# Kernel optimization log

Hardware: AMD Instinct MI355X
Metric: run time of the kernel (lower is better)

Reference implementation:

```python
import jax, jax.numpy as jnp
import numpy as np

B, H, V, NS, S, D, E = 4096, 256, 32000, 2, 128, 4, 64
PAD = 0


def _shift_matrices(n):
    # W_up: row i <- row i+1, last row zero. W_down: row i <- row i-1, row 0 zero.
    eye = np.eye(n, dtype=np.float32)
    W_up = np.vstack([eye[1:], np.zeros((1, n), np.float32)])
    W_down = np.vstack([np.zeros((1, n), np.float32), eye[:-1]])
    return W_up, W_down


def setup_inputs() -> dict:
    key = jax.random.key(0)
    ks = jax.random.split(key, 20)
    sc = 0.05
    emb_table = jax.random.normal(ks[0], (V, H), jnp.float32) * sc
    emb_table = emb_table.at[PAD].set(0.0)  # padding_idx
    inp = {
        "input_ids": jax.random.randint(ks[1], (B,), 0, V),
        "hidden": jax.random.normal(ks[2], (B, H), jnp.float32),
        "stacks": jax.random.normal(ks[3], (B, NS, S, E), jnp.float32),
        "emb_table": emb_table,
        "W_in": jax.random.normal(ks[4], (H, H), jnp.float32) * sc,
        "b_in": jnp.zeros((H,), jnp.float32),
        "W_hh": jax.random.normal(ks[5], (H, H), jnp.float32) * sc,
        "b_hh": jnp.zeros((H,), jnp.float32),
        "W_s2h": jax.random.normal(ks[6], (NS, H, D * E), jnp.float32) * sc,
        "b_s2h": jnp.zeros((NS, H), jnp.float32),
        "W_act": jax.random.normal(ks[7], (NS, 3, H), jnp.float32) * sc,
        "b_act": jnp.zeros((NS, 3), jnp.float32),
        "W_push": jax.random.normal(ks[8], (NS, E, H), jnp.float32) * sc,
        "b_push": jnp.zeros((NS, E), jnp.float32),
        "W_out": jax.random.normal(ks[9], (V, H), jnp.float32) * sc,
        "b_out": jnp.zeros((V,), jnp.float32),
        "empty_elem": jax.random.normal(ks[10], (1, E), jnp.float32),
    }
    return inp


def reference(input_ids, hidden, stacks, emb_table, W_in, b_in, W_hh, b_hh,
              W_s2h, b_s2h, W_act, b_act, W_push, b_push, W_out, b_out,
              empty_elem):
    W_up_np, W_down_np = _shift_matrices(S)
    W_up = jnp.asarray(W_up_np)
    W_down = jnp.asarray(W_down_np)

    emb = emb_table[input_ids]                                  # [B,H]
    mid = emb @ W_in.T + b_in + hidden @ W_hh.T + b_hh          # [B,H]

    # stack readout (top stack_depth elems), before any update
    stack_vals = stacks[:, :, :D, :].reshape(B, NS, D * E)      # [B,NS,D*E]
    mid = mid + jnp.einsum('bnd,nhd->bh', stack_vals, W_s2h) + b_s2h.sum(0)

    # per-stack actions from the OLD hidden state (no softmax in source)
    act = jnp.einsum('bh,nah->bna', hidden, W_act) + b_act      # [B,NS,3]
    p_push = act[..., 0:1]                                      # [B,NS,1]
    p_pop = act[..., 1:2]
    p_noop = act[..., 2:3]
    push_val = jnp.tanh(jnp.einsum('bh,neh->bne', hidden, W_push) + b_push)  # [B,NS,E]

    down = jnp.einsum('st,bnte->bnse', W_down, stacks)          # shift down
    up = jnp.einsum('st,bnte->bnse', W_up, stacks)              # shift up
    new_stacks = (p_push[..., None] * down + p_pop[..., None] * up
                  + p_noop[..., None] * stacks)
    new_stacks = new_stacks.at[:, :, 0, :].set(p_push * push_val)
    new_stacks = new_stacks.at[:, :, S - 1, :].set(
        jnp.broadcast_to(empty_elem[None], (B, NS, E)))

    new_hidden = jnp.tanh(mid)                                  # [B,H]
    logits = new_hidden @ W_out.T + b_out                       # [B,V]
    output = jax.nn.log_softmax(logits, axis=1)
    top1 = jnp.argmax(output, axis=1)[:, None]                  # [B,1]
    return output, new_hidden, top1, new_stacks
```

## Files before the change

kernel.cpp:

```cpp
#include <hip/hip_runtime.h>
#include <stdint.h>

#define B_   4096
#define H_   256
#define V_   32000
#define NS_  2
#define S_   128
#define E_   64
#define TRIG 0.02f
#define CSTR 10
#define NTV  500

typedef __attribute__((ext_vector_type(4))) float  f32x4;
typedef __attribute__((ext_vector_type(8))) __bf16 bf16x8;
typedef __attribute__((ext_vector_type(8))) unsigned short u16x8;

__device__ __forceinline__ unsigned short f2bf(float f) {
  unsigned u = __float_as_uint(f);
  u += 0x7fffu + ((u >> 16) & 1u);
  return (unsigned short)(u >> 16);
}

typedef __attribute__((address_space(1))) const unsigned int* gas1_t;
typedef __attribute__((address_space(3))) unsigned int*       las3_t;
__device__ __forceinline__ void gload16(const void* g, void* l) {
  __builtin_amdgcn_global_load_lds((gas1_t)g, (las3_t)l, 16, 0, 0);
}

__device__ __forceinline__ void merge2(float& m1, float& i1, float& m2, float& i2,
                                       float om1, float oi1, float om2, float oi2) {
  if (om1 > m1 || (om1 == m1 && oi1 < i1)) {
    const float lm = m1, li = i1;
    m1 = om1; i1 = oi1;
    if (lm > om2 || (lm == om2 && li < oi2)) { m2 = lm; i2 = li; }
    else { m2 = om2; i2 = oi2; }
  } else {
    if (om1 > m2 || (om1 == m2 && oi1 < i2)) { m2 = om1; i2 = oi1; }
  }
}

__global__ void prep_w1(const float* __restrict__ W_in,  const float* __restrict__ W_hh,
                        const float* __restrict__ W_s2h, const float* __restrict__ W_act,
                        const float* __restrict__ W_push,
                        const float* __restrict__ b_in,  const float* __restrict__ b_hh,
                        const float* __restrict__ b_s2h, const float* __restrict__ b_act,
                        const float* __restrict__ b_push,
                        unsigned short* __restrict__ W1, float* __restrict__ bbig) {
  const unsigned idx = blockIdx.x * 256u + threadIdx.x;
  const unsigned c = idx >> 10, k = idx & 1023u;
  float w = 0.f;
  if (c < 256u) {
    if (k < 256u)       w = W_in[c*256u + k];
    else if (k < 512u)  w = W_hh[c*256u + (k-256u)];
    else { unsigned n = (k-512u) >> 8, d = (k-512u) & 255u; w = W_s2h[n*65536u + c*256u + d]; }
  } else if (c < 262u) {
    if (k >= 256u && k < 512u) w = W_act[(c-256u)*256u + (k-256u)];
  } else if (c < 390u) {
    if (k >= 256u && k < 512u) w = W_push[(c-262u)*256u + (k-256u)];
  }
  W1[(size_t)c*1024u + k] = f2bf(w);
  if (idx < 512u) {
    float bb = 0.f;
    if (idx < 256u)       bb = b_in[idx] + b_hh[idx] + b_s2h[idx] + b_s2h[256u+idx];
    else if (idx < 262u)  bb = b_act[idx-256u];
    else if (idx < 390u)  bb = b_push[idx-262u];
    bbig[idx] = bb;
  }
}

__global__ void prep_w1t(const float* __restrict__ W_in, const float* __restrict__ W_hh,
                         const float* __restrict__ W_s2h, float* __restrict__ W1T) {
  const unsigned idx = blockIdx.x * 256u + threadIdx.x;
  const unsigned k = idx >> 8, h = idx & 255u;
  float w;
  if (k < 256u)      w = W_in[h*256u + k];
  else if (k < 512u) w = W_hh[h*256u + (k-256u)];
  else { unsigned n = (k-512u) >> 8, d = (k-512u) & 255u; w = W_s2h[n*65536u + h*256u + d]; }
  W1T[idx] = w;
}

__global__ void prep_a1(const int* __restrict__ ids, const float* __restrict__ emb,
                        const float* __restrict__ hidden, const float* __restrict__ stacks,
                        unsigned short* __restrict__ A1, float* __restrict__ A1f) {
  const unsigned gid = blockIdx.x * 256u + threadIdx.x;
  const unsigned b = gid >> 7, k0 = (gid & 127u) << 3;
  const float* src;
  if (k0 < 256u)      src = emb + (size_t)ids[b]*256u + k0;
  else if (k0 < 512u) src = hidden + (size_t)b*256u + (k0-256u);
  else { const unsigned kk = k0 - 512u;
         src = stacks + (size_t)b*16384u + (kk>>8)*8192u + (kk&255u); }
  const float4 v0 = *(const float4*)src;
  const float4 v1 = *(const float4*)(src + 4);
  *(float4*)(A1f + (size_t)b*1024u + k0)     = v0;
  *(float4*)(A1f + (size_t)b*1024u + k0 + 4) = v1;
  u16x8 o;
  o[0]=f2bf(v0.x); o[1]=f2bf(v0.y); o[2]=f2bf(v0.z); o[3]=f2bf(v0.w);
  o[4]=f2bf(v1.x); o[5]=f2bf(v1.y); o[6]=f2bf(v1.z); o[7]=f2bf(v1.w);
  *(u16x8*)(A1 + (size_t)b*1024u + k0) = o;
}

__global__ void prep_b2(const float* __restrict__ W_out, unsigned short* __restrict__ B2) {
  const unsigned gid = blockIdx.x * 256u + threadIdx.x;
  const size_t base = (size_t)gid * 8;
  const float4 v0 = *(const float4*)(W_out + base);
  const float4 v1 = *(const float4*)(W_out + base + 4);
  u16x8 o;
  o[0]=f2bf(v0.x); o[1]=f2bf(v0.y); o[2]=f2bf(v0.z); o[3]=f2bf(v0.w);
  o[4]=f2bf(v1.x); o[5]=f2bf(v1.y); o[6]=f2bf(v1.z); o[7]=f2bf(v1.w);
  *(u16x8*)(B2 + base) = o;
}

__global__ __launch_bounds__(256) void gemm_mid(
    const unsigned short* __restrict__ A, const unsigned short* __restrict__ Bm,
    float* __restrict__ nh_out, float* __restrict__ actw, float* __restrict__ pushw,
    const float* __restrict__ bbig, unsigned short* __restrict__ a2w)
{
  constexpr int K = 1024;
  constexpr int NT = K >> 6;
  __shared__ __align__(16) unsigned char pool[65536];
  const int tid  = threadIdx.x;
  const int lane = tid & 63;
  const int wid  = tid >> 6;
  const int wm = wid >> 1, wn = wid & 1;
  const int l16 = lane & 15;
  const int lk8 = (lane >> 4) << 3;
  const int lr4 = (lane >> 4) << 2;
  const size_t arow0 = (size_t)blockIdx.y << 7;
  const size_t bcol0 = (size_t)blockIdx.x << 7;

  f32x4 acc[4][4];
#pragma unroll
  for (int i = 0; i < 4; ++i)
#pragma unroll
    for (int j = 0; j < 4; ++j) acc[i][j] = (f32x4)0.f;

  auto stageAB = [&](int buf, int kt) {
    unsigned char* dst = pool + (buf << 15);
    const int k0 = kt << 6;
#pragma unroll
    for (int i = 0; i < 4; ++i) {
      const int e   = (i << 8) + tid;
      const int row = e >> 3;
      const int col = (e & 7) << 3;
      gload16(A  + (arow0 + row) * (size_t)K + (k0 + col), dst + (size_t)e * 16);
      gload16(Bm + (bcol0 + row) * (size_t)K + (k0 + col), dst + 16384 + (size_t)e * 16);
    }
  };
  auto computeT = [&](int buf) {
    const unsigned short* As = (const unsigned short*)(pool + (buf << 15));
    const unsigned short* Bs = As + 8192;
#pragma unroll
    for (int kk = 0; kk < 64; kk += 32) {
      bf16x8 af[4], bfr[4];
#pragma unroll
      for (int f = 0; f < 4; ++f) {
        af[f]  = *(const bf16x8*)&As[((wm<<6) + (f<<4) + l16)*64 + kk + lk8];
        bfr[f] = *(const bf16x8*)&Bs[((wn<<6) + (f<<4) + l16)*64 + kk + lk8];
      }
#pragma unroll
      for (int mf = 0; mf < 4; ++mf)
#pragma unroll
        for (int nf = 0; nf < 4; ++nf)
          acc[mf][nf] = __builtin_amdgcn_mfma_f32_16x16x32_bf16(af[mf], bfr[nf], acc[mf][nf], 0, 0, 0);
    }
  };

  stageAB(0, 0);
  __syncthreads();
#pragma unroll
  for (int t = 0; t < NT; ++t) {
    if (t < NT - 1) stageAB((t + 1) & 1, t + 1);
    computeT(t & 1);
    __syncthreads();
  }

#pragma unroll
  for (int mf = 0; mf < 4; ++mf)
#pragma unroll
    for (int j = 0; j < 4; ++j) {
      const int r = (int)arow0 + (wm<<6) + (mf<<4) + lr4 + j;
#pragma unroll
      for (int nf = 0; nf < 4; ++nf) {
        const int c = (int)bcol0 + (wn<<6) + (nf<<4) + l16;
        const float v = acc[mf][nf][j] + bbig[c];
        if (c < 256) { const float th = tanhf(v);
                       nh_out[r*256 + c] = th;
                       a2w[r*256 + c] = f2bf(th); }
        else if (c < 262)  actw[r*6 + (c-256)] = v;
        else if (c < 390)  pushw[r*128 + (c-262)] = tanhf(v);
      }
    }
}

template<int MODE>
__global__ __launch_bounds__(512, 4) void gemmBS(
    const unsigned short* __restrict__ A2, const unsigned short* __restrict__ B2,
    float* __restrict__ gout, const float* __restrict__ b_out,
    float* __restrict__ partials, const float* __restrict__ subw)
{
  __shared__ __align__(16) unsigned short Bres[64*256];
  __shared__ __align__(16) unsigned short Apool[2][256*32];
  __shared__ __align__(16) float tscr[2112];
  const int tid  = threadIdx.x;
  const int lane = tid & 63;
  const int wid  = tid >> 6;
  const int wm = wid >> 2;
  const int wn = wid & 3;
  const int l16 = lane & 15;
  const int g4  = lane >> 4;
  const int lr4 = g4 << 2;
  const int vb  = (int)blockIdx.x << 6;

  {
#pragma unroll
    for (int i = 0; i < 4; ++i) {
      const int e   = (i << 9) + tid;
      const int row = e >> 5;
      const int c32 = e & 31;
      const int src = (c32 & 24) | ((c32 ^ row) & 7);
      gload16(B2 + (size_t)(vb + row) * 256 + (src << 3),
              (unsigned char*)Bres + (size_t)e * 16);
    }
  }

  auto stageA = [&](int buf, int bt, int kt) {
    unsigned char* dst = (unsigned char*)Apool[buf];
#pragma unroll
    for (int i = 0; i < 2; ++i) {
      const int e   = (i << 9) + tid;
      const int row = e >> 2;
      const int src = (e & 3) ^ ((row >> 2) & 3);
      gload16(A2 + ((size_t)bt*256 + row) * 256 + kt*32 + (src << 3),
              dst + (size_t)e * 16);
    }
  };

  stageA(0, 0, 0);
  __syncthreads();

  for (int bt = 0; bt < 16; ++bt) {
    f32x4 acc[2][4];
#pragma unroll
    for (int m = 0; m < 2; ++m)
#pragma unroll
      for (int n = 0; n < 4; ++n) acc[m][n] = (f32x4)0.f;

#pragma unroll
    for (int kt = 0; kt < 8; ++kt) {
      if (kt < 7)       stageA((kt + 1) & 1, bt, kt + 1);
      else if (bt < 15) stageA(0, bt + 1, 0);
      {
        const unsigned short* As = Apool[kt & 1];
        bf16x8 af[2], bfr[4];
#pragma unroll
        for (int m = 0; m < 2; ++m) {
          const int rb = (wm<<5) + (m<<4) + l16;
          const int ch = kt*4 + g4;
          const int s  = (ch & 24) | ((ch ^ rb) & 7);
          af[m] = *(const bf16x8*)&Bres[rb*256 + (s<<3)];
        }
#pragma unroll
        for (int n = 0; n < 4; ++n) {
          const int ra = (wn<<6) + (n<<4) + l16;
          const int s  = g4 ^ ((ra >> 2) & 3);
          bfr[n] = *(const bf16x8*)&As[ra*32 + (s<<3)];
        }
#pragma unroll
        for (int m = 0; m < 2; ++m)
#pragma unroll
          for (int n = 0; n < 4; ++n)
            acc[m][n] = __builtin_amdgcn_mfma_f32_16x16x32_bf16(af[m], bfr[n], acc[m][n], 0, 0, 0);
      }
      __syncthreads();
    }

    if constexpr (MODE == 0) {
      float* lf = tscr;
#pragma unroll
      for (int ch = 0; ch < 8; ++ch) {
        if (wn == (ch >> 1)) {
          const int nb = (ch & 1) << 1;
#pragma unroll
          for (int mm = 0; mm < 2; ++mm)
#pragma unroll
            for (int nn = 0; nn < 2; ++nn) {
              const int brow = (nn << 4) + l16;
              const int vcol = (wm << 5) + (mm << 4) + lr4;
#pragma unroll
              for (int j = 0; j < 4; ++j)
                lf[brow*66 + vcol + j] = acc[mm][nb + nn][j];
            }
        }
        __syncthreads();
        {
          const int r  = tid >> 4;
          const int c4 = (tid & 15) << 2;
          const size_t grow = (size_t)bt*256 + (ch << 5) + r;
          const float ls = subw[grow];
          const f32x4 bo = *(const f32x4*)&b_out[vb + c4];
          f32x4 v;
          v.x = lf[r*66 + c4 + 0] + bo.x - ls;
          v.y = lf[r*66 + c4 + 1] + bo.y - ls;
          v.z = lf[r*66 + c4 + 2] + bo.z - ls;
          v.w = lf[r*66 + c4 + 3] + bo.w - ls;
          __builtin_nontemporal_store(v, (f32x4*)(gout + grow * (size_t)V_ + vb + c4));
        }
        __syncthreads();
      }
    } else {
      float (*colrec)[5] = (float (*)[5])tscr;
      float bo[8];
#pragma unroll
      for (int m = 0; m < 2; ++m)
#pragma unroll
        for (int j = 0; j < 4; ++j)
          bo[m*4+j] = b_out[vb + (wm<<5) + (m<<4) + lr4 + j];

      float rS[4], rM1[4], rI1[4], rM2[4], rI2[4];
#pragma unroll
      for (int n = 0; n < 4; ++n) {
        float s = 0.f, m1 = -INFINITY, i1f = 2.1e9f, m2 = -INFINITY, i2f = 2.1e9f;
#pragma unroll
        for (int m = 0; m < 2; ++m)
#pragma unroll
          for (int j = 0; j < 4; ++j) {
            const int vloc = (wm<<5) + (m<<4) + lr4 + j;
            const float v = acc[m][n][j] + bo[m*4+j];
            const float fi = (float)(vb + vloc);
            s += __expf(v);
            if (v > m1 || (v == m1 && fi < i1f)) { m2 = m1; i2f = i1f; m1 = v; i1f = fi; }
            else if (v > m2 || (v == m2 && fi < i2f)) { m2 = v; i2f = fi; }
          }
#pragma unroll
        for (int mask = 16; mask <= 32; mask <<= 1) {
          const float os  = __shfl_xor(s,   mask, 64);
          const float om1 = __shfl_xor(m1,  mask, 64);
          const float oi1 = __shfl_xor(i1f, mask, 64);
          const float om2 = __shfl_xor(m2,  mask, 64);
          const float oi2 = __shfl_xor(i2f, mask, 64);
          s += os;
          merge2(m1, i1f, m2, i2f, om1, oi1, om2, oi2);
        }
        rS[n] = s; rM1[n] = m1; rI1[n] = i1f; rM2[n] = m2; rI2[n] = i2f;
      }
      if (wm == 0 && g4 == 0) {
#pragma unroll
        for (int n = 0; n < 4; ++n) {
          const int cl = (wn<<6) + (n<<4) + l16;
          colrec[cl][0] = rS[n];  colrec[cl][1] = rM1[n]; colrec[cl][2] = rI1[n];
          colrec[cl][3] = rM2[n]; colrec[cl][4] = rI2[n];
        }
      }
      __syncthreads();
      if (wm == 1 && g4 == 0) {
#pragma unroll
        for (int n = 0; n < 4; ++n) {
          const int cl = (wn<<6) + (n<<4) + l16;
          float s = rS[n] + colrec[cl][0];
          float m1 = rM1[n], i1f = rI1[n], m2 = rM2[n], i2f = rI2[n];
          merge2(m1, i1f, m2, i2f, colrec[cl][1], colrec[cl][2], colrec[cl][3], colrec[cl][4]);
          const size_t brow = (size_t)bt*256 + cl;
          float* dst = partials + (brow * NTV + blockIdx.x) * 8;
          float4 v4; v4.x = s; v4.y = m1; v4.z = i1f; v4.w = m2;
          *(float4*)dst = v4;
          dst[4] = i2f;
        }
      }
      __syncthreads();
    }
  }
}

__global__ __launch_bounds__(256) void reduce_kernel(
    const float* __restrict__ partials, float* __restrict__ subw,
    float* __restrict__ top1w, int* __restrict__ candbuf)
{
  const int b = blockIdx.x, t = threadIdx.x;
  float s = 0.f, m1 = -INFINITY, i1 = 2.1e9f, m2 = -INFINITY, i2 = 2.1e9f;
  float tm1[2] = {-INFINITY,-INFINITY}, ti1[2] = {2.1e9f,2.1e9f};
  float tm2[2] = {-INFINITY,-INFINITY}, ti2[2] = {2.1e9f,2.1e9f};
  for (int q = 0; q < 2; ++q) {
    const int idx = t + q*256;
    if (idx < NTV) {
      const float4 p0 = *(const float4*)(partials + ((size_t)b*NTV + idx)*8);
      s += p0.x;
      tm1[q] = p0.y; ti1[q] = p0.z; tm2[q] = p0.w;
      ti2[q] = partials[((size_t)b*NTV + idx)*8 + 4];
      merge2(m1, i1, m2, i2, tm1[q], ti1[q], tm2[q], ti2[q]);
    }
  }
  __shared__ float sS[256], sM1[256], sI1[256], sM2[256], sI2[256];
  sS[t] = s; sM1[t] = m1; sI1[t] = i1; sM2[t] = m2; sI2[t] = i2;
  __syncthreads();
  for (int off = 128; off > 0; off >>= 1) {
    if (t < off) {
      sS[t] += sS[t+off];
      float a1 = sM1[t], ai1 = sI1[t], a2 = sM2[t], ai2 = sI2[t];
      merge2(a1, ai1, a2, ai2, sM1[t+off], sI1[t+off], sM2[t+off], sI2[t+off]);
      sM1[t] = a1; sI1[t] = ai1; sM2[t] = a2; sI2[t] = ai2;
    }
    __syncthreads();
  }
  const float M1 = sM1[0];
  __shared__ int cnt; __shared__ int cand[CSTR-1];
  if (t == 0) cnt = 0;
  __syncthreads();
  for (int q = 0; q < 2; ++q) {
    if (t + q*256 < NTV) {
      if (tm1[q] >= M1 - TRIG) { int p = atomicAdd(&cnt, 1); if (p < CSTR-1) cand[p] = (int)ti1[q]; }
      if (tm2[q] >= M1 - TRIG) { int p = atomicAdd(&cnt, 1); if (p < CSTR-1) cand[p] = (int)ti2[q]; }
    }
  }
  __syncthreads();
  const int ncand = min(cnt, CSTR-1);
  if (t == 0) {
    subw[b] = logf(sS[0]);
    candbuf[b*CSTR] = ncand;
    if (ncand <= 1) top1w[b] = sI1[0];
  }
  if (t < ncand) candbuf[b*CSTR + 1 + t] = cand[t];
}

__global__ __launch_bounds__(256) void rescue_kernel(
    const int* __restrict__ candbuf, const float* __restrict__ A1f,
    const float* __restrict__ W1T, const float* __restrict__ bbig,
    const float* __restrict__ W_out, const float* __restrict__ b_out,
    float* __restrict__ top1w)
{
  const int b = blockIdx.x;
  const int ncand = candbuf[b*CSTR];
  if (ncand <= 1) return;
  const int t = threadIdx.x;

  double acc = (double)bbig[t];
  const float* arow = A1f + (size_t)b * 1024;
  for (int k = 0; k < 1024; ++k)
    acc += (double)arow[k] * (double)W1T[k*256 + t];
  __shared__ double hbuf[256];
  hbuf[t] = tanh(acc);
  __syncthreads();

  __shared__ double red[256];
  double best = -1e300; int besti = 0x7fffffff;
  for (int q = 0; q < ncand; ++q) {
    const int ci = candbuf[b*CSTR + 1 + q];
    red[t] = hbuf[t] * (double)W_out[(size_t)ci*256 + t];
    __syncthreads();
    for (int off = 128; off > 0; off >>= 1) {
      if (t < off) red[t] += red[t+off];
      __syncthreads();
    }
    if (t == 0) {
      const double d = red[0] + (double)b_out[ci];
      if (d > best || (d == best && ci < besti)) { best = d; besti = ci; }
    }
    __syncthreads();
  }
  if (t == 0) top1w[b] = (float)besti;
}

__global__ void stacks_kernel(const float* __restrict__ stacks, const float* __restrict__ actw,
                              const float* __restrict__ pushw, const float* __restrict__ empty,
                              float* __restrict__ out3) {
  const int bn = blockIdx.x;
  const int b = bn >> 1, n = bn & 1;
  __shared__ __align__(16) float st[S_*E_];
  const float4* src4 = (const float4*)(stacks + (size_t)bn * (S_*E_));
  float4* st4 = (float4*)st;
  for (int i = threadIdx.x; i < (S_*E_/4); i += 256) st4[i] = src4[i];
  __syncthreads();
  const float pp = actw[b*6 + n*3 + 0];
  const float po = actw[b*6 + n*3 + 1];
  const float pq = actw[b*6 + n*3 + 2];
  float4* dst4 = (float4*)(out3 + (size_t)bn * (S_*E_));
  for (int i = threadIdx.x; i < (S_*E_/4); i += 256) {
    const int flat = i << 2;
    const int s = flat >> 6;
    const int e = flat & 63;
    float4 r;
    if (s == S_-1) {
      r = ((const float4*)empty)[e >> 2];
    } else if (s == 0) {
      const float4 pv = ((const float4*)(pushw + b*128 + n*64))[e >> 2];
      r.x = pp*pv.x; r.y = pp*pv.y; r.z = pp*pv.z; r.w = pp*pv.w;
    } else {
      const float4 dn = *(const float4*)&st[(s-1)*64 + e];
      const float4 up = *(const float4*)&st[(s+1)*64 + e];
      const float4 cu = *(const float4*)&st[s*64 + e];
      r.x = pp*dn.x + po*up.x + pq*cu.x;
      r.y = pp*dn.y + po*up.y + pq*cu.y;
      r.z = pp*dn.z + po*up.z + pq*cu.z;
      r.w = pp*dn.w + po*up.w + pq*cu.w;
    }
    dst4[i] = r;
  }
}

extern "C" void kernel_launch(void* const* d_in, const int* in_sizes, int n_in,
                              void* d_out, int out_size, void* d_ws, size_t ws_size,
                              hipStream_t stream) {
  (void)in_sizes; (void)n_in; (void)out_size; (void)ws_size;
  const int*   ids    = (const int*)  d_in[0];
  const float* hidden = (const float*)d_in[1];
  const float* stacks = (const float*)d_in[2];
  const float* emb    = (const float*)d_in[3];
  const float* W_in   = (const float*)d_in[4];
  const float* b_in   = (const float*)d_in[5];
  const float* W_hh   = (const float*)d_in[6];
  const float* b_hh   = (const float*)d_in[7];
  const float* W_s2h  = (const float*)d_in[8];
  const float* b_s2h  = (const float*)d_in[9];
  const float* W_act  = (const float*)d_in[10];
  const float* b_act  = (const float*)d_in[11];
  const float* W_push = (const float*)d_in[12];
  const float* b_push = (const float*)d_in[13];
  const float* W_out  = (const float*)d_in[14];
  const float* b_out  = (const float*)d_in[15];
  const float* empty  = (const float*)d_in[16];

  float* out0 = (float*)d_out;
  float* out1 = out0 + (size_t)B_*V_;
  float* out2 = out1 + (size_t)B_*H_;
  float* out3 = out2 + B_;

  unsigned short* A1 = (unsigned short*)out3;
  unsigned short* W1 = A1 + (size_t)4194304;
  unsigned short* A2 = W1 + (size_t)524288;
  unsigned short* B2 = A2 + (size_t)1048576;
  float* partials    = (float*)(B2 + (size_t)8192000);
  float* A1f         = partials + (size_t)16384000;
  float* W1T         = A1f + (size_t)4194304;
  int*   candbuf     = (int*)(W1T + 262144);

  float* bbig  = (float*)d_ws;
  float* actw  = bbig + 512;
  float* pushw = actw + (size_t)B_*6;
  float* subw  = pushw + (size_t)B_*128;

  prep_w1<<<dim3(2048),  dim3(256), 0, stream>>>(W_in, W_hh, W_s2h, W_act, W_push,
                                                 b_in, b_hh, b_s2h, b_act, b_push, W1, bbig);
  prep_w1t<<<dim3(1024), dim3(256), 0, stream>>>(W_in, W_hh, W_s2h, W1T);
  prep_a1<<<dim3(2048),  dim3(256), 0, stream>>>(ids, emb, hidden, stacks, A1, A1f);
  gemm_mid<<<dim3(4, 32), dim3(256), 0, stream>>>(A1, W1, out1, actw, pushw, bbig, A2);
  prep_b2<<<dim3(4000),  dim3(256), 0, stream>>>(W_out, B2);
  gemmBS<2><<<dim3(500), dim3(512), 0, stream>>>(A2, B2,
      nullptr, b_out, partials, nullptr);
  reduce_kernel<<<dim3(4096), dim3(256), 0, stream>>>(partials, subw, out2, candbuf);
  gemmBS<0><<<dim3(500), dim3(512), 0, stream>>>(A2, B2,
      out0, b_out, nullptr, subw);
  rescue_kernel<<<dim3(4096), dim3(256), 0, stream>>>(candbuf, A1f, W1T, bbig,
                                                      W_out, b_out, out2);
  stacks_kernel<<<dim3(8192), dim3(256), 0, stream>>>(stacks, actw, pushw, empty, out3);
}
```

Baseline: 540.2 us.

## Restructure vocab GEMM so each wave owns full vocab tile and loads A directly

The warp tiling of the output-projection GEMM changes. Each wave now covers all 64 vocab columns for 32 batch rows, so no cross-wave reduction is needed. The activation operand is read straight from global memory into registers with one-step prefetch, replacing the LDS double buffer and its per-k-step barriers. The MODE 0 epilogue writes accumulators directly, without the LDS transpose, and MODE 1 drops the LDS combine of the two wave halves. In exchange, each wave does uncoalesced 16-byte global loads of A with more redundant A traffic through cache, the occupancy hint drops from 4 to 2, and the output stores are less contiguous.

```diff
diff --git a/kernel.cpp b/kernel.cpp
--- a/kernel.cpp
+++ b/kernel.cpp
@@ -193,23 +193,19 @@
 }
 
 template<int MODE>
-__global__ __launch_bounds__(512, 4) void gemmBS(
+__global__ __launch_bounds__(512, 2) void gemmBS(
     const unsigned short* __restrict__ A2, const unsigned short* __restrict__ B2,
     float* __restrict__ gout, const float* __restrict__ b_out,
     float* __restrict__ partials, const float* __restrict__ subw)
 {
   __shared__ __align__(16) unsigned short Bres[64*256];
-  __shared__ __align__(16) unsigned short Apool[2][256*32];
-  __shared__ __align__(16) float tscr[2112];
   const int tid  = threadIdx.x;
   const int lane = tid & 63;
-  const int wid  = tid >> 6;
-  const int wm = wid >> 2;
-  const int wn = wid & 3;
-  const int l16 = lane & 15;
-  const int g4  = lane >> 4;
-  const int lr4 = g4 << 2;
-  const int vb  = (int)blockIdx.x << 6;
+  const int w    = tid >> 6;
+  const int l16  = lane & 15;
+  const int g4   = lane >> 4;
+  const int lr4  = g4 << 2;
+  const int vb   = (int)blockIdx.x << 6;
 
   {
 #pragma unroll
@@ -222,111 +218,75 @@
               (unsigned char*)Bres + (size_t)e * 16);
     }
   }
-
-  auto stageA = [&](int buf, int bt, int kt) {
-    unsigned char* dst = (unsigned char*)Apool[buf];
-#pragma unroll
-    for (int i = 0; i < 2; ++i) {
-      const int e   = (i << 9) + tid;
-      const int row = e >> 2;
-      const int src = (e & 3) ^ ((row >> 2) & 3);
-      gload16(A2 + ((size_t)bt*256 + row) * 256 + kt*32 + (src << 3),
-              dst + (size_t)e * 16);
-    }
-  };
-
-  stageA(0, 0, 0);
-  __syncthreads();
+  __syncthreads();
+
+  f32x4 bo4[4];
+#pragma unroll
+  for (int m = 0; m < 4; ++m)
+    bo4[m] = *(const f32x4*)&b_out[vb + (m<<4) + lr4];
 
   for (int bt = 0; bt < 16; ++bt) {
-    f32x4 acc[2][4];
-#pragma unroll
-    for (int m = 0; m < 2; ++m)
-#pragma unroll
-      for (int n = 0; n < 4; ++n) acc[m][n] = (f32x4)0.f;
-
+    f32x4 acc[4][2];
+#pragma unroll
+    for (int m = 0; m < 4; ++m)
+#pragma unroll
+      for (int n = 0; n < 2; ++n) acc[m][n] = (f32x4)0.f;
+
+    const unsigned short* Abase = A2 + ((size_t)bt*256) * 256;
+
+    bf16x8 pb[2];
+#pragma unroll
+    for (int n = 0; n < 2; ++n) {
+      const int ra = (w<<5) + (n<<4) + l16;
+      pb[n] = *(const bf16x8*)&Abase[(size_t)ra*256 + (g4<<3)];
+    }
 #pragma unroll
     for (int kt = 0; kt < 8; ++kt) {
-      if (kt < 7)       stageA((kt + 1) & 1, bt, kt + 1);
-      else if (bt < 15) stageA(0, bt + 1, 0);
-      {
-        const unsigned short* As = Apool[kt & 1];
-        bf16x8 af[2], bfr[4];
-#pragma unroll
-        for (int m = 0; m < 2; ++m) {
-          const int rb = (wm<<5) + (m<<4) + l16;
-          const int ch = kt*4 + g4;
-          const int s  = (ch & 24) | ((ch ^ rb) & 7);
-          af[m] = *(const bf16x8*)&Bres[rb*256 + (s<<3)];
+      bf16x8 cb0 = pb[0], cb1 = pb[1];
+      if (kt < 7) {
+#pragma unroll
+        for (int n = 0; n < 2; ++n) {
+          const int ra = (w<<5) + (n<<4) + l16;
+          pb[n] = *(const bf16x8*)&Abase[(size_t)ra*256 + (kt+1)*32 + (g4<<3)];
         }
-#pragma unroll
-        for (int n = 0; n < 4; ++n) {
-          const int ra = (wn<<6) + (n<<4) + l16;
-          const int s  = g4 ^ ((ra >> 2) & 3);
-          bfr[n] = *(const bf16x8*)&As[ra*32 + (s<<3)];
+      }
+      bf16x8 af[4];
+#pragma unroll
+      for (int m = 0; m < 4; ++m) {
+        const int rb = (m<<4) + l16;
+        const int ch = kt*4 + g4;
+        const int s  = (ch & 24) | ((ch ^ rb) & 7);
+        af[m] = *(const bf16x8*)&Bres[rb*256 + (s<<3)];
+      }
+#pragma unroll
+      for (int m = 0; m < 4; ++m) {
+        acc[m][0] = __builtin_amdgcn_mfma_f32_16x16x32_bf16(af[m], cb0, acc[m][0], 0, 0, 0);
+        acc[m][1] = __builtin_amdgcn_mfma_f32_16x16x32_bf16(af[m], cb1, acc[m][1], 0, 0, 0);
+      }
+    }
+
+    if constexpr (MODE == 0) {
+#pragma unroll
+      for (int n = 0; n < 2; ++n) {
+        const size_t grow = (size_t)bt*256 + (w<<5) + (n<<4) + l16;
+        const float ls = subw[grow];
+        float* gp = gout + grow * (size_t)V_ + vb + lr4;
+#pragma unroll
+        for (int m = 0; m < 4; ++m) {
+          f32x4 v = acc[m][n] + bo4[m] - ls;
+          __builtin_nontemporal_store(v, (f32x4*)(gp + (m<<4)));
         }
-#pragma unroll
-        for (int m = 0; m < 2; ++m)
-#pragma unroll
-          for (int n = 0; n < 4; ++n)
-            acc[m][n] = __builtin_amdgcn_mfma_f32_16x16x32_bf16(af[m], bfr[n], acc[m][n], 0, 0, 0);
-      }
-      __syncthreads();
-    }
-
-    if constexpr (MODE == 0) {
-      float* lf = tscr;
-#pragma unroll
-      for (int ch = 0; ch < 8; ++ch) {
-        if (wn == (ch >> 1)) {
-          const int nb = (ch & 1) << 1;
-#pragma unroll
-          for (int mm = 0; mm < 2; ++mm)
-#pragma unroll
-            for (int nn = 0; nn < 2; ++nn) {
-              const int brow = (nn << 4) + l16;
-              const int vcol = (wm << 5) + (mm << 4) + lr4;
-#pragma unroll
-              for (int j = 0; j < 4; ++j)
-                lf[brow*66 + vcol + j] = acc[mm][nb + nn][j];
-            }
-        }
-        __syncthreads();
-        {
-          const int r  = tid >> 4;
-          const int c4 = (tid & 15) << 2;
-          const size_t grow = (size_t)bt*256 + (ch << 5) + r;
-          const float ls = subw[grow];
-          const f32x4 bo = *(const f32x4*)&b_out[vb + c4];
-          f32x4 v;
-          v.x = lf[r*66 + c4 + 0] + bo.x - ls;
-          v.y = lf[r*66 + c4 + 1] + bo.y - ls;
-          v.z = lf[r*66 + c4 + 2] + bo.z - ls;
-          v.w = lf[r*66 + c4 + 3] + bo.w - ls;
-          __builtin_nontemporal_store(v, (f32x4*)(gout + grow * (size_t)V_ + vb + c4));
-        }
-        __syncthreads();
       }
     } else {
-      float (*colrec)[5] = (float (*)[5])tscr;
-      float bo[8];
-#pragma unroll
-      for (int m = 0; m < 2; ++m)
-#pragma unroll
-        for (int j = 0; j < 4; ++j)
-          bo[m*4+j] = b_out[vb + (wm<<5) + (m<<4) + lr4 + j];
-
-      float rS[4], rM1[4], rI1[4], rM2[4], rI2[4];
-#pragma unroll
-      for (int n = 0; n < 4; ++n) {
+#pragma unroll
+      for (int n = 0; n < 2; ++n) {
         float s = 0.f, m1 = -INFINITY, i1f = 2.1e9f, m2 = -INFINITY, i2f = 2.1e9f;
 #pragma unroll
-        for (int m = 0; m < 2; ++m)
+        for (int m = 0; m < 4; ++m)
 #pragma unroll
           for (int j = 0; j < 4; ++j) {
-            const int vloc = (wm<<5) + (m<<4) + lr4 + j;
-            const float v = acc[m][n][j] + bo[m*4+j];
-            const float fi = (float)(vb + vloc);
+            const float v = acc[m][n][j] + bo4[m][j];
+            const float fi = (float)(vb + (m<<4) + lr4 + j);
             s += __expf(v);
             if (v > m1 || (v == m1 && fi < i1f)) { m2 = m1; i2f = i1f; m1 = v; i1f = fi; }
             else if (v > m2 || (v == m2 && fi < i2f)) { m2 = v; i2f = fi; }
@@ -341,32 +301,14 @@
           s += os;
           merge2(m1, i1f, m2, i2f, om1, oi1, om2, oi2);
         }
-        rS[n] = s; rM1[n] = m1; rI1[n] = i1f; rM2[n] = m2; rI2[n] = i2f;
-      }
-      if (wm == 0 && g4 == 0) {
-#pragma unroll
-        for (int n = 0; n < 4; ++n) {
-          const int cl = (wn<<6) + (n<<4) + l16;
-          colrec[cl][0] = rS[n];  colrec[cl][1] = rM1[n]; colrec[cl][2] = rI1[n];
-          colrec[cl][3] = rM2[n]; colrec[cl][4] = rI2[n];
-        }
-      }
-      __syncthreads();
-      if (wm == 1 && g4 == 0) {
-#pragma unroll
-        for (int n = 0; n < 4; ++n) {
-          const int cl = (wn<<6) + (n<<4) + l16;
-          float s = rS[n] + colrec[cl][0];
-          float m1 = rM1[n], i1f = rI1[n], m2 = rM2[n], i2f = rI2[n];
-          merge2(m1, i1f, m2, i2f, colrec[cl][1], colrec[cl][2], colrec[cl][3], colrec[cl][4]);
-          const size_t brow = (size_t)bt*256 + cl;
+        if (g4 == 0) {
+          const size_t brow = (size_t)bt*256 + (w<<5) + (n<<4) + l16;
           float* dst = partials + (brow * NTV + blockIdx.x) * 8;
           float4 v4; v4.x = s; v4.y = m1; v4.z = i1f; v4.w = m2;
           *(float4*)dst = v4;
           dst[4] = i2f;
         }
       }
-      __syncthreads();
     }
   }
 }
```

Measured after the change: 597.2 us. 1.11x slower.

## Split stats GEMM into dedicated kernel reading A2 from a k-major copy

Applied to the files above, without the earlier changes.

Splits the stats pass out of the templated logits GEMM into its own kernel, gemmStats. A new prep kernel copies the bf16 hidden activations into a k-chunk-major layout (A2F). gemmStats loads the B tile once into LDS, then streams A fragments straight from global memory into registers with one step of prefetch, with no A staging in LDS and no cross-wave merge. Each wave covers all 64 vocab columns for 32 batch rows, so the LDS colrec merge and its barriers go away. The cost is an extra small kernel launch, an extra buffer, and global-memory latency exposure on the A loads.

```diff
diff --git a/kernel.cpp b/kernel.cpp
--- a/kernel.cpp
+++ b/kernel.cpp
@@ -110,6 +110,13 @@
   *(u16x8*)(B2 + base) = o;
 }
 
+__global__ void prep_a2f(const unsigned short* __restrict__ A2,
+                         unsigned short* __restrict__ A2F) {
+  const unsigned gid = blockIdx.x * 256u + threadIdx.x;
+  const unsigned row = gid & 4095u, k8 = gid >> 12;
+  *(u16x8*)(A2F + (size_t)gid * 8) = *(const u16x8*)(A2 + (size_t)row*256u + k8*8u);
+}
+
 __global__ __launch_bounds__(256) void gemm_mid(
     const unsigned short* __restrict__ A, const unsigned short* __restrict__ Bm,
     float* __restrict__ nh_out, float* __restrict__ actw, float* __restrict__ pushw,
@@ -192,11 +199,10 @@
     }
 }
 
-template<int MODE>
-__global__ __launch_bounds__(512, 4) void gemmBS(
+__global__ __launch_bounds__(512, 4) void gemmW(
     const unsigned short* __restrict__ A2, const unsigned short* __restrict__ B2,
     float* __restrict__ gout, const float* __restrict__ b_out,
-    float* __restrict__ partials, const float* __restrict__ subw)
+    const float* __restrict__ subw)
 {
   __shared__ __align__(16) unsigned short Bres[64*256];
   __shared__ __align__(16) unsigned short Apool[2][256*32];
@@ -274,99 +280,139 @@
       __syncthreads();
     }
 
-    if constexpr (MODE == 0) {
-      float* lf = tscr;
-#pragma unroll
-      for (int ch = 0; ch < 8; ++ch) {
-        if (wn == (ch >> 1)) {
-          const int nb = (ch & 1) << 1;
-#pragma unroll
-          for (int mm = 0; mm < 2; ++mm)
-#pragma unroll
-            for (int nn = 0; nn < 2; ++nn) {
-              const int brow = (nn << 4) + l16;
-              const int vcol = (wm << 5) + (mm << 4) + lr4;
-#pragma unroll
-              for (int j = 0; j < 4; ++j)
-                lf[brow*66 + vcol + j] = acc[mm][nb + nn][j];
-            }
+#pragma unroll
+    for (int ch = 0; ch < 8; ++ch) {
+      if (wn == (ch >> 1)) {
+        const int nb = (ch & 1) << 1;
+#pragma unroll
+        for (int mm = 0; mm < 2; ++mm)
+#pragma unroll
+          for (int nn = 0; nn < 2; ++nn) {
+            const int brow = (nn << 4) + l16;
+            const int vcol = (wm << 5) + (mm << 4) + lr4;
+#pragma unroll
+            for (int j = 0; j < 4; ++j)
+              tscr[brow*66 + vcol + j] = acc[mm][nb + nn][j];
+          }
+      }
+      __syncthreads();
+      {
+        const int r  = tid >> 4;
+        const int c4 = (tid & 15) << 2;
+        const size_t grow = (size_t)bt*256 + (ch << 5) + r;
+        const float ls = subw[grow];
+        const f32x4 bo = *(const f32x4*)&b_out[vb + c4];
+        f32x4 v;
+        v.x = tscr[r*66 + c4 + 0] + bo.x - ls;
+        v.y = tscr[r*66 + c4 + 1] + bo.y - ls;
+        v.z = tscr[r*66 + c4 + 2] + bo.z - ls;
+        v.w = tscr[r*66 + c4 + 3] + bo.w - ls;
+        __builtin_nontemporal_store(v, (f32x4*)(gout + grow * (size_t)V_ + vb + c4));
+      }
+      __syncthreads();
+    }
+  }
+}
+
+__global__ __launch_bounds__(512, 4) void gemmStats(
+    const unsigned short* __restrict__ A2F, const unsigned short* __restrict__ B2,
+    const float* __restrict__ b_out, float* __restrict__ partials)
+{
+  __shared__ __align__(16) unsigned short Bres[64*256];
+  const int tid  = threadIdx.x;
+  const int lane = tid & 63;
+  const int w    = tid >> 6;
+  const int l16  = lane & 15;
+  const int g4   = lane >> 4;
+  const int lr4  = g4 << 2;
+  const int vb   = (int)blockIdx.x << 6;
+
+  {
+#pragma unroll
+    for (int i = 0; i < 4; ++i) {
+      const int e   = (i << 9) + tid;
+      const int row = e >> 5;
+      const int c32 = e & 31;
+      const int src = (c32 & 24) | ((c32 ^ row) & 7);
+      gload16(B2 + (size_t)(vb + row) * 256 + (src << 3),
+              (unsigned char*)Bres + (size_t)e * 16);
+    }
+  }
+  __syncthreads();
+
+  f32x4 bo4[4];
+#pragma unroll
+  for (int m = 0; m < 4; ++m)
+    bo4[m] = *(const f32x4*)&b_out[vb + (m<<4) + lr4];
+
+  for (int bt = 0; bt < 16; ++bt) {
+    f32x4 acc[4][2];
+#pragma unroll
+    for (int m = 0; m < 4; ++m)
+#pragma unroll
+      for (int n = 0; n < 2; ++n) acc[m][n] = (f32x4)0.f;
+
+    const int ra0 = (w<<5) + l16;
+
+    bf16x8 pb[2];
+#pragma unroll
+    for (int n = 0; n < 2; ++n)
+      pb[n] = *(const bf16x8*)&A2F[((size_t)g4*4096 + bt*256 + ra0 + (n<<4)) * 8];
+
+#pragma unroll
+    for (int kt = 0; kt < 8; ++kt) {
+      bf16x8 cb0 = pb[0], cb1 = pb[1];
+      if (kt < 7) {
+        const size_t k8 = (size_t)((kt+1)*4 + g4);
+#pragma unroll
+        for (int n = 0; n < 2; ++n)
+          pb[n] = *(const bf16x8*)&A2F[(k8*4096 + bt*256 + ra0 + (n<<4)) * 8];
+      }
+      bf16x8 af[4];
+#pragma unroll
+      for (int m = 0; m < 4; ++m) {
+        const int rb = (m<<4) + l16;
+        const int ch = kt*4 + g4;
+        const int s  = (ch & 24) | ((ch ^ rb) & 7);
+        af[m] = *(const bf16x8*)&Bres[rb*256 + (s<<3)];
+      }
+#pragma unroll
+      for (int m = 0; m < 4; ++m) {
+        acc[m][0] = __builtin_amdgcn_mfma_f32_16x16x32_bf16(af[m], cb0, acc[m][0], 0, 0, 0);
+        acc[m][1] = __builtin_amdgcn_mfma_f32_16x16x32_bf16(af[m], cb1, acc[m][1], 0, 0, 0);
+      }
+    }
+
+#pragma unroll
+    for (int n = 0; n < 2; ++n) {
+      float s = 0.f, m1 = -INFINITY, i1f = 2.1e9f, m2 = -INFINITY, i2f = 2.1e9f;
+#pragma unroll
+      for (int m = 0; m < 4; ++m)
+#pragma unroll
+        for (int j = 0; j < 4; ++j) {
+          const float v = acc[m][n][j] + bo4[m][j];
+          const float fi = (float)(vb + (m<<4) + lr4 + j);
+          s += __expf(v);
+          if (v > m1 || (v == m1 && fi < i1f)) { m2 = m1; i2f = i1f; m1 = v; i1f = fi; }
+          else if (v > m2 || (v == m2 && fi < i2f)) { m2 = v; i2f = fi; }
         }
-        __syncthreads();
-        {
-          const int r  = tid >> 4;
-          const int c4 = (tid & 15) << 2;
-          const size_t grow = (size_t)bt*256 + (ch << 5) + r;
-          const float ls = subw[grow];
-          const f32x4 bo = *(const f32x4*)&b_out[vb + c4];
-          f32x4 v;
-          v.x = lf[r*66 + c4 + 0] + bo.x - ls;
-          v.y = lf[r*66 + c4 + 1] + bo.y - ls;
-          v.z = lf[r*66 + c4 + 2] + bo.z - ls;
-          v.w = lf[r*66 + c4 + 3] + bo.w - ls;
-          __builtin_nontemporal_store(v, (f32x4*)(gout + grow * (size_t)V_ + vb + c4));
-        }
-        __syncthreads();
-      }
-    } else {
-      float (*colrec)[5] = (float (*)[5])tscr;
-      float bo[8];
-#pragma unroll
-      for (int m = 0; m < 2; ++m)
-#pragma unroll
-        for (int j = 0; j < 4; ++j)
-          bo[m*4+j] = b_out[vb + (wm<<5) + (m<<4) + lr4 + j];
-
-      float rS[4], rM1[4], rI1[4], rM2[4], rI2[4];
-#pragma unroll
-      for (int n = 0; n < 4; ++n) {
-        float s = 0.f, m1 = -INFINITY, i1f = 2.1e9f, m2 = -INFINITY, i2f = 2.1e9f;
-#pragma unroll
-        for (int m = 0; m < 2; ++m)
-#pragma unroll
-          for (int j = 0; j < 4; ++j) {
-            const int vloc = (wm<<5) + (m<<4) + lr4 + j;
-            const float v = acc[m][n][j] + bo[m*4+j];
-            const float fi = (float)(vb + vloc);
-            s += __expf(v);
-            if (v > m1 || (v == m1 && fi < i1f)) { m2 = m1; i2f = i1f; m1 = v; i1f = fi; }
-            else if (v > m2 || (v == m2 && fi < i2f)) { m2 = v; i2f = fi; }
-          }
-#pragma unroll
-        for (int mask = 16; mask <= 32; mask <<= 1) {
-          const float os  = __shfl_xor(s,   mask, 64);
-          const float om1 = __shfl_xor(m1,  mask, 64);
-          const float oi1 = __shfl_xor(i1f, mask, 64);
-          const float om2 = __shfl_xor(m2,  mask, 64);
-          const float oi2 = __shfl_xor(i2f, mask, 64);
-          s += os;
-          merge2(m1, i1f, m2, i2f, om1, oi1, om2, oi2);
-        }
-        rS[n] = s; rM1[n] = m1; rI1[n] = i1f; rM2[n] = m2; rI2[n] = i2f;
-      }
-      if (wm == 0 && g4 == 0) {
-#pragma unroll
-        for (int n = 0; n < 4; ++n) {
-          const int cl = (wn<<6) + (n<<4) + l16;
-          colrec[cl][0] = rS[n];  colrec[cl][1] = rM1[n]; colrec[cl][2] = rI1[n];
-          colrec[cl][3] = rM2[n]; colrec[cl][4] = rI2[n];
-        }
-      }
-      __syncthreads();
-      if (wm == 1 && g4 == 0) {
-#pragma unroll
-        for (int n = 0; n < 4; ++n) {
-          const int cl = (wn<<6) + (n<<4) + l16;
-          float s = rS[n] + colrec[cl][0];
-          float m1 = rM1[n], i1f = rI1[n], m2 = rM2[n], i2f = rI2[n];
-          merge2(m1, i1f, m2, i2f, colrec[cl][1], colrec[cl][2], colrec[cl][3], colrec[cl][4]);
-          const size_t brow = (size_t)bt*256 + cl;
-          float* dst = partials + (brow * NTV + blockIdx.x) * 8;
-          float4 v4; v4.x = s; v4.y = m1; v4.z = i1f; v4.w = m2;
-          *(float4*)dst = v4;
-          dst[4] = i2f;
-        }
-      }
-      __syncthreads();
+#pragma unroll
+      for (int mask = 16; mask <= 32; mask <<= 1) {
+        const float os  = __shfl_xor(s,   mask, 64);
+        const float om1 = __shfl_xor(m1,  mask, 64);
+        const float oi1 = __shfl_xor(i1f, mask, 64);
+        const float om2 = __shfl_xor(m2,  mask, 64);
+        const float oi2 = __shfl_xor(i2f, mask, 64);
+        s += os;
+        merge2(m1, i1f, m2, i2f, om1, oi1, om2, oi2);
+      }
+      if (g4 == 0) {
+        const size_t brow = (size_t)bt*256 + (w<<5) + (n<<4) + l16;
+        float* dst = partials + (brow * NTV + blockIdx.x) * 8;
+        float4 v4; v4.x = s; v4.y = m1; v4.z = i1f; v4.w = m2;
+        *(float4*)dst = v4;
+        dst[4] = i2f;
+      }
     }
   }
 }
@@ -531,6 +577,7 @@
   float* A1f         = partials + (size_t)16384000;
   float* W1T         = A1f + (size_t)4194304;
   int*   candbuf     = (int*)(W1T + 262144);
+  unsigned short* A2F = (unsigned short*)(candbuf + 4096*CSTR);
 
   float* bbig  = (float*)d_ws;
   float* actw  = bbig + 512;
@@ -543,11 +590,10 @@
   prep_a1<<<dim3(2048),  dim3(256), 0, stream>>>(ids, emb, hidden, stacks, A1, A1f);
   gemm_mid<<<dim3(4, 32), dim3(256), 0, stream>>>(A1, W1, out1, actw, pushw, bbig, A2);
   prep_b2<<<dim3(4000),  dim3(256), 0, stream>>>(W_out, B2);
-  gemmBS<2><<<dim3(500), dim3(512), 0, stream>>>(A2, B2,
-      nullptr, b_out, partials, nullptr);
+  prep_a2f<<<dim3(512),  dim3(256), 0, stream>>>(A2, A2F);
+  gemmStats<<<dim3(500), dim3(512), 0, stream>>>(A2F, B2, b_out, partials);
   reduce_kernel<<<dim3(4096), dim3(256), 0, stream>>>(partials, subw, out2, candbuf);
-  gemmBS<0><<<dim3(500), dim3(512), 0, stream>>>(A2, B2,
-      out0, b_out, nullptr, subw);
+  gemmW<<<dim3(500), dim3(512), 0, stream>>>(A2, B2, out0, b_out, subw);
   rescue_kernel<<<dim3(4096), dim3(256), 0, stream>>>(candbuf, A1f, W1T, bbig,
                                                       W_out, b_out, out2);
   stacks_kernel<<<dim3(8192), dim3(256), 0, stream>>>(stacks, actw, pushw, empty, out3);
```

Result: slower. 764.6 us (+41.5%).
